# Performance work log

Measured on AMD Instinct MI355X. Metric: run time of the kernel, lower is better.

## Reference

```python
import jax, jax.numpy as jnp
import numpy as np

N, B, NUM_NODES, D_IN = 16384, 16, 1024, 1024
H, C = 4, 128
E = 262144


def _g(k, shape, fan_in):
    return jax.random.normal(k, shape, jnp.float32) * (1.0 / np.sqrt(fan_in))


def setup_inputs() -> dict:
    key = jax.random.key(0)
    ks = jax.random.split(key, 32)
    HC = H * C
    inp = {
        'x': jax.random.normal(ks[0], (N, D_IN), jnp.float32),
        'edge_index': jax.random.randint(ks[1], (2, E), 0, N, dtype=jnp.int64),
        'batch': jnp.repeat(jnp.arange(B, dtype=jnp.int64), NUM_NODES),
        # GATConv 1 (D_IN -> H x C, concat)
        'W1': _g(ks[2], (D_IN, HC), D_IN),
        'att_src1': _g(ks[3], (H, C), C),
        'att_dst1': _g(ks[4], (H, C), C),
        'b1': jnp.zeros((HC,), jnp.float32),
        # GATConv 2 (H*C -> H x C, concat)
        'W2': _g(ks[5], (HC, HC), HC),
        'att_src2': _g(ks[6], (H, C), C),
        'att_dst2': _g(ks[7], (H, C), C),
        'b2': jnp.zeros((HC,), jnp.float32),
        # pooling linears (HC -> 1)
        'p1w': _g(ks[8], (HC, 1), HC), 'p1b': jnp.zeros((1,), jnp.float32),
        'p2w': _g(ks[9], (HC, 1), HC), 'p2b': jnp.zeros((1,), jnp.float32),
        # layer_norm0 (applied to x2 per original code)
        'ln_g': jnp.ones((NUM_NODES,), jnp.float32),
        'ln_b': jnp.zeros((NUM_NODES,), jnp.float32),
        # encoder MLP 1024->512->256->128->64, last 64->1
        'fw1': _g(ks[10], (NUM_NODES, 512), NUM_NODES), 'fb1': jnp.zeros((512,), jnp.float32),
        'fw2': _g(ks[11], (512, 256), 512), 'fb2': jnp.zeros((256,), jnp.float32),
        'fw3': _g(ks[12], (256, 128), 256), 'fb3': jnp.zeros((128,), jnp.float32),
        'fw4': _g(ks[13], (128, 64), 128), 'fb4': jnp.zeros((64,), jnp.float32),
        'lw': _g(ks[14], (64, 1), 64), 'lb': jnp.zeros((1,), jnp.float32),
    }
    return inp


def gat_conv(x, src, dst, W, a_src, a_dst, b):
    # x: [N, F_in] -> h: [N, H, C]
    h = (x @ W).reshape(N, H, C)
    alpha_src = jnp.sum(h * a_src[None], axis=-1)  # [N, H]
    alpha_dst = jnp.sum(h * a_dst[None], axis=-1)  # [N, H]
    e = jax.nn.leaky_relu(alpha_src[src] + alpha_dst[dst], 0.2)  # [E', H]
    # segment softmax over destination neighborhoods (every node has a self loop)
    emax = jax.ops.segment_max(e, dst, num_segments=N)
    ex = jnp.exp(e - emax[dst])
    denom = jax.ops.segment_sum(ex, dst, num_segments=N)
    alpha = ex / (denom[dst] + 1e-16)  # [E', H]
    msg = h[src] * alpha[:, :, None]  # [E', H, C]
    out = jax.ops.segment_sum(msg, dst, num_segments=N)  # [N, H, C]
    return out.reshape(N, H * C) + b


def layer_norm(x, g, b, eps=1e-5):
    mu = jnp.mean(x, axis=-1, keepdims=True)
    var = jnp.var(x, axis=-1, keepdims=True)
    return (x - mu) * jax.lax.rsqrt(var + eps) * g + b


def reference(x, edge_index, batch, W1, att_src1, att_dst1, b1, W2, att_src2, att_dst2, b2,
              p1w, p1b, p2w, p2b, ln_g, ln_b, fw1, fb1, fw2, fb2, fw3, fb3, fw4, fb4, lw, lb):
    # add self loops (GATConv default)
    loops = jnp.arange(N, dtype=edge_index.dtype)
    src = jnp.concatenate([edge_index[0], loops])
    dst = jnp.concatenate([edge_index[1], loops])

    h1 = jax.nn.elu(gat_conv(x, src, dst, W1, att_src1, att_dst1, b1))
    # pool1 + to_dense_batch: batch is sorted with NUM_NODES nodes per graph -> reshape
    x1 = (h1 @ p1w + p1b).squeeze(-1).reshape(B, NUM_NODES)
    h2 = jax.nn.elu(gat_conv(h1, src, dst, W2, att_src2, att_dst2, b2))
    x2 = (h2 @ p2w + p2b).squeeze(-1).reshape(B, NUM_NODES)

    # opt.layer_norm=True; original bug: x2 normalized by layer_norm0
    x2 = layer_norm(x2, ln_g, ln_b)
    multiscale = x2  # which_layer == 'layer3'

    e = jax.nn.elu(multiscale @ fw1 + fb1)
    e = jax.nn.elu(e @ fw2 + fb2)
    e = jax.nn.elu(e @ fw3 + fb3)
    e = jax.nn.elu(e @ fw4 + fb4)
    pred = e @ lw + lb  # act_type='none' -> no activation
    return multiscale, e, pred
```

## Files before the change

kernel.cpp:

```cpp
#include <hip/hip_runtime.h>
#include <math.h>

#define NN    16384
#define DIN   1024
#define HCdim 512
#define NHEAD 4
#define NE_   262144
#define EP_   (NE_ + NN)

using short8  = __attribute__((ext_vector_type(8))) short;
using floatx4 = __attribute__((ext_vector_type(4))) float;

typedef __attribute__((address_space(3))) unsigned int lds_uint;
typedef const __attribute__((address_space(1))) unsigned int glb_uint;
#define ASYNC_LD16(g, l) __builtin_amdgcn_global_load_lds((glb_uint*)(g), (lds_uint*)(l), 16, 0, 0)

__device__ __forceinline__ float eluf(float x){ return x > 0.f ? x : expm1f(x); }
__device__ __forceinline__ float lrelu(float x){ return x > 0.f ? x : 0.2f * x; }
__device__ __forceinline__ float bf2f(unsigned short u){
    union { unsigned int i; float f; } c; c.i = ((unsigned int)u) << 16; return c.f;
}
__device__ __forceinline__ unsigned short f2b(float f){
    union { float f; unsigned int u; } c; c.f = f;
    unsigned int u = c.u;
    return (unsigned short)((u + 0x7FFFu + ((u >> 16) & 1u)) >> 16);
}

__global__ void k_zero_i(int* __restrict__ p, int n){
    int i = blockIdx.x * 256 + threadIdx.x;
    if (i < n) p[i] = 0;
}

__global__ void k_degree(const int* __restrict__ ei, int* __restrict__ deg){
    int i = blockIdx.x * 256 + threadIdx.x;
    if (i >= EP_) return;
    int d = (i < NE_) ? ei[NE_ + i] : (i - NE_);
    atomicAdd(&deg[d], 1);
}

__global__ __launch_bounds__(1024) void k_scan(const int* __restrict__ deg, int* __restrict__ offs){
    __shared__ int s[1024];
    int tid  = threadIdx.x;
    int base = tid * 16;
    int local[16];
    int sum = 0;
    #pragma unroll
    for (int i = 0; i < 16; i++){ local[i] = deg[base + i]; sum += local[i]; }
    s[tid] = sum;
    __syncthreads();
    for (int off = 1; off < 1024; off <<= 1){
        int v = (tid >= off) ? s[tid - off] : 0;
        __syncthreads();
        s[tid] += v;
        __syncthreads();
    }
    int run = (tid == 0) ? 0 : s[tid - 1];
    #pragma unroll
    for (int i = 0; i < 16; i++){ offs[base + i] = run; run += local[i]; }
    if (tid == 1023) offs[NN] = run;
}

__global__ void k_scatter(const int* __restrict__ ei, const int* __restrict__ offs,
                          int* __restrict__ cursor, int* __restrict__ csr){
    int i = blockIdx.x * 256 + threadIdx.x;
    if (i >= EP_) return;
    int srcv, dstv;
    if (i < NE_){ srcv = ei[i]; dstv = ei[NE_ + i]; }
    else        { srcv = dstv = i - NE_; }
    int pos = offs[dstv] + atomicAdd(&cursor[dstv], 1);
    csr[pos] = srcv;
}

__global__ __launch_bounds__(256) void k_casts(const float* __restrict__ x, ushort* __restrict__ xb,
    const float* __restrict__ W1, ushort* __restrict__ W1T,
    const float* __restrict__ W2, ushort* __restrict__ W2T){
    int bid = blockIdx.x, tid = threadIdx.x;
    if (bid < 16384){
        int i = bid * 256 + tid;
        float4 v = *(const float4*)(x + (size_t)i * 4);
        ushort4 o = { f2b(v.x), f2b(v.y), f2b(v.z), f2b(v.w) };
        *(ushort4*)(xb + (size_t)i * 4) = o;
    } else if (bid < 16384 + 512){
        int t = (bid - 16384) * 256 + tid;
        int n = t >> 8, kb = (t & 255) * 4;
        ushort4 o = { f2b(W1[(size_t)(kb+0)*HCdim + n]), f2b(W1[(size_t)(kb+1)*HCdim + n]),
                      f2b(W1[(size_t)(kb+2)*HCdim + n]), f2b(W1[(size_t)(kb+3)*HCdim + n]) };
        *(ushort4*)(W1T + (size_t)n * DIN + kb) = o;
    } else {
        int t = (bid - 16896) * 256 + tid;
        int n = t >> 7, kb = (t & 127) * 4;
        ushort4 o = { f2b(W2[(size_t)(kb+0)*HCdim + n]), f2b(W2[(size_t)(kb+1)*HCdim + n]),
                      f2b(W2[(size_t)(kb+2)*HCdim + n]), f2b(W2[(size_t)(kb+3)*HCdim + n]) };
        *(ushort4*)(W2T + (size_t)n * HCdim + kb) = o;
    }
}

__global__ __launch_bounds__(256) void gemm_bf16(const ushort* __restrict__ A,
                                                 const ushort* __restrict__ BT,
                                                 ushort* __restrict__ C,
                                                 const float* __restrict__ att_s,
                                                 const float* __restrict__ att_d,
                                                 float* __restrict__ as_, float* __restrict__ ad_,
                                                 int M, int Nn, int K){
    __shared__ ushort As[128 * 32];
    __shared__ ushort Bs[128 * 32];
    __shared__ float prS[2][128];
    __shared__ float prD[2][128];
    int tid = threadIdx.x;
    int m0 = blockIdx.y * 128, n0 = blockIdx.x * 128;
    int cx = blockIdx.x;
    int lane = tid & 63, w = tid >> 6;
    int wm = (w >> 1) * 64, wn = (w & 1) * 64;
    int la = lane & 15, qd = lane >> 4;

    int srow = tid >> 2, schunk = (tid & 3) * 8;
    const ushort* Ag = A  + (size_t)(m0 + srow) * K + schunk;
    const ushort* Bg = BT + (size_t)(n0 + srow) * K + schunk;
    ushort* Asw = &As[srow * 32 + schunk];
    ushort* Bsw = &Bs[srow * 32 + schunk];

    floatx4 acc[4][4] = {};
    for (int k0 = 0; k0 < K; k0 += 32){
        __syncthreads();
        ASYNC_LD16(Ag + k0,                  Asw);
        ASYNC_LD16(Ag + (size_t)64 * K + k0, Asw + 64 * 32);
        ASYNC_LD16(Bg + k0,                  Bsw);
        ASYNC_LD16(Bg + (size_t)64 * K + k0, Bsw + 64 * 32);
        __syncthreads();
        short8 af[4], bf[4];
        #pragma unroll
        for (int i = 0; i < 4; i++){
            af[i] = *(const short8*)&As[(wm + i*16 + la) * 32 + qd * 8];
            bf[i] = *(const short8*)&Bs[(wn + i*16 + la) * 32 + qd * 8];
        }
        #pragma unroll
        for (int i = 0; i < 4; i++)
            #pragma unroll
            for (int j = 0; j < 4; j++)
                acc[i][j] = __builtin_amdgcn_mfma_f32_16x16x32_bf16(af[i], bf[j], acc[i][j], 0, 0, 0);
    }
    float asv[4], adv[4];
    #pragma unroll
    for (int j = 0; j < 4; j++){
        asv[j] = att_s[cx * 128 + wn + j * 16 + la];
        adv[j] = att_d[cx * 128 + wn + j * 16 + la];
    }
    int half = wn >> 6;
    #pragma unroll
    for (int i = 0; i < 4; i++){
        #pragma unroll
        for (int r = 0; r < 4; r++){
            float ps = 0.f, pd = 0.f;
            #pragma unroll
            for (int j = 0; j < 4; j++){
                ps = fmaf(acc[i][j][r], asv[j], ps);
                pd = fmaf(acc[i][j][r], adv[j], pd);
            }
            #pragma unroll
            for (int off = 1; off < 16; off <<= 1){
                ps += __shfl_xor(ps, off);
                pd += __shfl_xor(pd, off);
            }
            if (la == 0){
                int rl = wm + i * 16 + qd * 4 + r;
                prS[half][rl] = ps; prD[half][rl] = pd;
            }
        }
    }
    #pragma unroll
    for (int i = 0; i < 4; i++)
        #pragma unroll
        for (int j = 0; j < 4; j++){
            int col = n0 + wn + j * 16 + la;
            #pragma unroll
            for (int r = 0; r < 4; r++){
                int row = m0 + wm + i * 16 + qd * 4 + r;
                C[(size_t)row * Nn + col] = f2b(acc[i][j][r]);
            }
        }
    __syncthreads();
    if (tid < 128){
        as_[(size_t)(m0 + tid) * 4 + cx] = prS[0][tid] + prS[1][tid];
        ad_[(size_t)(m0 + tid) * 4 + cx] = prD[0][tid] + prD[1][tid];
    }
}

__global__ __launch_bounds__(256) void k_edgew(const int* __restrict__ offs, const int* __restrict__ csr,
    const float* __restrict__ as_, const float* __restrict__ ad_, ushort* __restrict__ wbuf){
    int wv = threadIdx.x >> 6, lane = threadIdx.x & 63;
    int n = blockIdx.x * 4 + wv;
    int start = offs[n], end = offs[n + 1];
    float4 ad4 = *(const float4*)(ad_ + (size_t)n * 4);
    for (int j = start + lane; j < end; j += 64){
        int s = csr[j];
        float4 as4 = *(const float4*)(as_ + (size_t)s * 4);
        ushort4 o = { f2b(__expf(lrelu(as4.x + ad4.x))), f2b(__expf(lrelu(as4.y + ad4.y))),
                      f2b(__expf(lrelu(as4.z + ad4.z))), f2b(__expf(lrelu(as4.w + ad4.w))) };
        *(ushort4*)(wbuf + (size_t)j * 4) = o;
    }
}

#define AGG_CONSUME(WS, HV)                                  \
    { float wgt = bf2f(WS);                                  \
      dsum += wgt;                                           \
      a0 = fmaf(wgt, bf2f(HV.x & 0xffff), a0);               \
      a1 = fmaf(wgt, bf2f(HV.x >> 16),    a1);               \
      a2 = fmaf(wgt, bf2f(HV.y & 0xffff), a2);               \
      a3 = fmaf(wgt, bf2f(HV.y >> 16),    a3);               \
      a4 = fmaf(wgt, bf2f(HV.z & 0xffff), a4);               \
      a5 = fmaf(wgt, bf2f(HV.z >> 16),    a5);               \
      a6 = fmaf(wgt, bf2f(HV.w & 0xffff), a6);               \
      a7 = fmaf(wgt, bf2f(HV.w >> 16),    a7); }

template<bool POOL>
__global__ __launch_bounds__(256) void k_aggregate(const ushort* __restrict__ h,
    const int* __restrict__ offs, const int* __restrict__ csr,
    const ushort* __restrict__ wbuf,
    const float* __restrict__ bias, ushort* __restrict__ out,
    const float* __restrict__ pw, const float* __restrict__ pb, float* __restrict__ x2){
    int wv   = threadIdx.x >> 6;
    int lane = threadIdx.x & 63;
    int n    = blockIdx.x * 4 + wv;
    int head = lane >> 4;
    int start = offs[n], end = offs[n + 1];
    float dsum = 0.f;
    float a0=0.f,a1=0.f,a2=0.f,a3=0.f,a4=0.f,a5=0.f,a6=0.f,a7=0.f;
    for (int base = start; base < end; base += 64){
        int cnt = min(64, end - base);
        int pre = (base + lane < end) ? csr[base + lane] : 0;
        int s0 = __builtin_amdgcn_readlane(pre, 0);
        ushort w0 = wbuf[(size_t)base * 4 + head];
        uint4  h0 = *(const uint4*)(h + (size_t)s0 * HCdim + lane * 8);
        ushort w1 = 0; uint4 h1 = {0,0,0,0};
        if (cnt > 1){
            int s1 = __builtin_amdgcn_readlane(pre, 1);
            w1 = wbuf[(size_t)(base + 1) * 4 + head];
            h1 = *(const uint4*)(h + (size_t)s1 * HCdim + lane * 8);
        }
        for (int jj = 0; jj < cnt; jj++){
            ushort w2 = 0; uint4 h2 = {0,0,0,0};
            if (jj + 2 < cnt){
                int s2 = __builtin_amdgcn_readlane(pre, jj + 2);
                w2 = wbuf[(size_t)(base + jj + 2) * 4 + head];
                h2 = *(const uint4*)(h + (size_t)s2 * HCdim + lane * 8);
            }
            AGG_CONSUME(w0, h0);
            w0 = w1; h0 = h1;
            w1 = w2; h1 = h2;
        }
    }
    float rden = 1.f / (dsum + 1e-16f);
    float4 b0 = *(const float4*)(bias + lane * 8);
    float4 b1 = *(const float4*)(bias + lane * 8 + 4);
    float e0 = eluf(fmaf(a0, rden, b0.x));
    float e1 = eluf(fmaf(a1, rden, b0.y));
    float e2 = eluf(fmaf(a2, rden, b0.z));
    float e3 = eluf(fmaf(a3, rden, b0.w));
    float e4 = eluf(fmaf(a4, rden, b1.x));
    float e5 = eluf(fmaf(a5, rden, b1.y));
    float e6 = eluf(fmaf(a6, rden, b1.z));
    float e7 = eluf(fmaf(a7, rden, b1.w));
    uint4 o;
    o.x = (unsigned)f2b(e0) | ((unsigned)f2b(e1) << 16);
    o.y = (unsigned)f2b(e2) | ((unsigned)f2b(e3) << 16);
    o.z = (unsigned)f2b(e4) | ((unsigned)f2b(e5) << 16);
    o.w = (unsigned)f2b(e6) | ((unsigned)f2b(e7) << 16);
    *(uint4*)(out + (size_t)n * HCdim + lane * 8) = o;
    if (POOL){
        float4 w0p = *(const float4*)(pw + lane * 8);
        float4 w1p = *(const float4*)(pw + lane * 8 + 4);
        float s = e0*w0p.x + e1*w0p.y + e2*w0p.z + e3*w0p.w
                + e4*w1p.x + e5*w1p.y + e6*w1p.z + e7*w1p.w;
        #pragma unroll
        for (int off = 32; off; off >>= 1) s += __shfl_down(s, off);
        if (lane == 0) x2[n] = s + pb[0];
    }
}

__global__ __launch_bounds__(256) void k_fc1_ln(const float* __restrict__ x2,
    const float* __restrict__ lng, const float* __restrict__ lnb,
    const float* __restrict__ W, const float* __restrict__ bias,
    float* __restrict__ outms, float* __restrict__ e1b){
    __shared__ float xs[1024];
    __shared__ float red[4][64];
    __shared__ float red2[8];
    __shared__ float stats[2];
    int tid = threadIdx.x;
    int b = blockIdx.y, c0 = blockIdx.x * 64;
    float4 v = *(const float4*)(x2 + b * 1024 + tid * 4);
    float s  = v.x + v.y + v.z + v.w;
    float sq = v.x * v.x + v.y * v.y + v.z * v.z + v.w * v.w;
    #pragma unroll
    for (int off = 32; off; off >>= 1){ s += __shfl_down(s, off); sq += __shfl_down(sq, off); }
    if ((tid & 63) == 0){ red2[(tid >> 6) * 2] = s; red2[(tid >> 6) * 2 + 1] = sq; }
    __syncthreads();
    if (tid == 0){
        float S  = red2[0] + red2[2] + red2[4] + red2[6];
        float SQ = red2[1] + red2[3] + red2[5] + red2[7];
        float mu  = S * (1.f / 1024.f);
        float var = SQ * (1.f / 1024.f) - mu * mu;
        stats[0] = mu; stats[1] = rsqrtf(var + 1e-5f);
    }
    __syncthreads();
    float mu = stats[0], r = stats[1];
    float4 g4  = *(const float4*)(lng + tid * 4);
    float4 bb4 = *(const float4*)(lnb + tid * 4);
    float4 o;
    o.x = (v.x - mu) * r * g4.x + bb4.x;
    o.y = (v.y - mu) * r * g4.y + bb4.y;
    o.z = (v.z - mu) * r * g4.z + bb4.z;
    o.w = (v.w - mu) * r * g4.w + bb4.w;
    *(float4*)&xs[tid * 4] = o;
    if (blockIdx.x == 0) *(float4*)(outms + b * 1024 + tid * 4) = o;
    __syncthreads();
    int tx = tid & 63, ty = tid >> 6;
    const float* wp = W + (size_t)(ty * 256) * 512 + c0 + tx;
    float a = 0.f;
    #pragma unroll 8
    for (int i = 0; i < 256; i++)
        a = fmaf(xs[ty * 256 + i], wp[(size_t)i * 512], a);
    red[ty][tx] = a;
    __syncthreads();
    if (ty == 0){
        float vv = red[0][tx] + red[1][tx] + red[2][tx] + red[3][tx] + bias[c0 + tx];
        e1b[b * 512 + c0 + tx] = eluf(vv);
    }
}

template<int K, int NOUT>
__global__ __launch_bounds__(256) void k_fc(const float* __restrict__ in,
    const float* __restrict__ W, const float* __restrict__ bias, float* __restrict__ outb){
    __shared__ float xs[K];
    __shared__ float red[4][64];
    int tid = threadIdx.x;
    int b = blockIdx.y, c0 = blockIdx.x * 64;
    int tx = tid & 63, ty = tid >> 6;
    for (int i = tid * 4; i < K; i += 1024)
        *(float4*)&xs[i] = *(const float4*)(in + b * K + i);
    __syncthreads();
    const float* wp = W + (size_t)(ty * (K / 4)) * NOUT + c0 + tx;
    float a = 0.f;
    #pragma unroll 8
    for (int i = 0; i < K / 4; i++)
        a = fmaf(xs[ty * (K / 4) + i], wp[(size_t)i * NOUT], a);
    red[ty][tx] = a;
    __syncthreads();
    if (ty == 0){
        float v = red[0][tx] + red[1][tx] + red[2][tx] + red[3][tx] + bias[c0 + tx];
        outb[b * NOUT + tx + c0] = eluf(v);
    }
}

__global__ __launch_bounds__(256) void k_fc_final(const float* __restrict__ in,
    const float* __restrict__ W, const float* __restrict__ bias,
    const float* __restrict__ lw, const float* __restrict__ lb, float* __restrict__ out){
    __shared__ float xs[128];
    __shared__ float red[4][64];
    __shared__ float evs[64];
    int tid = threadIdx.x;
    int b = blockIdx.x;
    int tx = tid & 63, ty = tid >> 6;
    if (tid * 4 < 128)
        *(float4*)&xs[tid * 4] = *(const float4*)(in + b * 128 + tid * 4);
    __syncthreads();
    const float* wp = W + (size_t)(ty * 32) * 64 + tx;
    float a = 0.f;
    #pragma unroll
    for (int i = 0; i < 32; i++)
        a = fmaf(xs[ty * 32 + i], wp[(size_t)i * 64], a);
    red[ty][tx] = a;
    __syncthreads();
    if (ty == 0){
        float ev = eluf(red[0][tx] + red[1][tx] + red[2][tx] + red[3][tx] + bias[tx]);
        evs[tx] = ev;
        out[16384 + b * 64 + tx] = ev;
    }
    __syncthreads();
    if (ty == 0){
        float p = evs[tx] * lw[tx];
        #pragma unroll
        for (int off = 32; off; off >>= 1) p += __shfl_down(p, off);
        if (tx == 0) out[16384 + 1024 + b] = p + lb[0];
    }
}

extern "C" void kernel_launch(void* const* d_in, const int* in_sizes, int n_in,
                              void* d_out, int out_size, void* d_ws, size_t ws_size,
                              hipStream_t stream) {
    const float* x        = (const float*)d_in[0];
    const int*   ei       = (const int*)  d_in[1];
    const float* W1       = (const float*)d_in[3];
    const float* att_src1 = (const float*)d_in[4];
    const float* att_dst1 = (const float*)d_in[5];
    const float* b1       = (const float*)d_in[6];
    const float* W2       = (const float*)d_in[7];
    const float* att_src2 = (const float*)d_in[8];
    const float* att_dst2 = (const float*)d_in[9];
    const float* b2       = (const float*)d_in[10];
    const float* p2w      = (const float*)d_in[13];
    const float* p2b      = (const float*)d_in[14];
    const float* ln_g     = (const float*)d_in[15];
    const float* ln_b     = (const float*)d_in[16];
    const float* fw1      = (const float*)d_in[17];
    const float* fb1      = (const float*)d_in[18];
    const float* fw2      = (const float*)d_in[19];
    const float* fb2      = (const float*)d_in[20];
    const float* fw3      = (const float*)d_in[21];
    const float* fb3      = (const float*)d_in[22];
    const float* fw4      = (const float*)d_in[23];
    const float* fb4      = (const float*)d_in[24];
    const float* lw       = (const float*)d_in[25];
    const float* lb       = (const float*)d_in[26];
    float* out = (float*)d_out;

    char* w = (char*)d_ws;
    ushort* xb   = (ushort*)(w);
    ushort* h1b  = (ushort*)(w);
    ushort* h2b  = (ushort*)(w + 16777216);
    ushort* hpre = (ushort*)(w + 33554432);
    ushort* W1T  = (ushort*)(w + 50331648);
    ushort* W2T  = (ushort*)(w + 51380224);
    float* asb   = (float*)(w + 51904512);
    float* adb   = (float*)(w + 52166656);
    int*   deg   = (int*)  (w + 52428800);
    int*   cursor= (int*)  (w + 52494336);
    int*   offs  = (int*)  (w + 52559872);
    int*   csr   = (int*)  (w + 52625664);
    ushort* wbuf = (ushort*)(w + 53739776);
    float* x2b   = (float*)(w + 55968000);
    float* e1b   = (float*)(w + 56033536);
    float* e2b   = (float*)(w + 56066304);
    float* e3b   = (float*)(w + 56082688);

    k_zero_i <<<(2 * NN + 255) / 256, 256, 0, stream>>>(deg, 2 * NN);
    k_degree <<<(EP_ + 255) / 256, 256, 0, stream>>>(ei, deg);
    k_scan   <<<1, 1024, 0, stream>>>(deg, offs);
    k_scatter<<<(EP_ + 255) / 256, 256, 0, stream>>>(ei, offs, cursor, csr);

    k_casts<<<16384 + 512 + 256, 256, 0, stream>>>(x, xb, W1, W1T, W2, W2T);

    dim3 ggrid(HCdim / 128, NN / 128);
    gemm_bf16         <<<ggrid, 256, 0, stream>>>(xb, W1T, hpre, att_src1, att_dst1,
                                                  asb, adb, NN, HCdim, DIN);
    k_edgew           <<<NN / 4, 256, 0, stream>>>(offs, csr, asb, adb, wbuf);
    k_aggregate<false><<<NN / 4, 256, 0, stream>>>(hpre, offs, csr, wbuf, b1, h1b,
                                                   nullptr, nullptr, nullptr);
    gemm_bf16         <<<ggrid, 256, 0, stream>>>(h1b, W2T, hpre, att_src2, att_dst2,
                                                  asb, adb, NN, HCdim, HCdim);
    k_edgew           <<<NN / 4, 256, 0, stream>>>(offs, csr, asb, adb, wbuf);
    k_aggregate<true> <<<NN / 4, 256, 0, stream>>>(hpre, offs, csr, wbuf, b2, h2b,
                                                   p2w, p2b, x2b);
    k_fc1_ln          <<<dim3(8, 16), 256, 0, stream>>>(x2b, ln_g, ln_b, fw1, fb1, out, e1b);
    k_fc< 512, 256>   <<<dim3(4, 16), 256, 0, stream>>>(e1b, fw2, fb2, e2b);
    k_fc< 256, 128>   <<<dim3(2, 16), 256, 0, stream>>>(e2b, fw3, fb3, e3b);
    k_fc_final        <<<16, 256, 0, stream>>>(e3b, fw4, fb4, lw, lb, out);
}
```

Before: 376.0 us.

## Split aggregation rows across two waves and deepen gather prefetch to eight edges

The GAT aggregation kernel now assigns two wavefronts per destination node, each covering half the 512 channels with 4 channels per lane, which doubles the grid. The gather loop is restructured into a double-buffered pipeline that keeps 4 to 8 neighbor loads in flight instead of 2. Out-of-range edges are clamped and given zero weight rather than branched around. The pooling reduction now combines the two half-row partials through shared memory with a block barrier. The aim is more memory-level parallelism for the irregular neighbor gathers, at the cost of narrower 8-byte loads and duplicated CSR and weight reads per node.

```diff
diff --git a/kernel.cpp b/kernel.cpp
--- a/kernel.cpp
+++ b/kernel.cpp
@@ -200,80 +200,75 @@
     }
 }
 
-#define AGG_CONSUME(WS, HV)                                  \
-    { float wgt = bf2f(WS);                                  \
-      dsum += wgt;                                           \
-      a0 = fmaf(wgt, bf2f(HV.x & 0xffff), a0);               \
-      a1 = fmaf(wgt, bf2f(HV.x >> 16),    a1);               \
-      a2 = fmaf(wgt, bf2f(HV.y & 0xffff), a2);               \
-      a3 = fmaf(wgt, bf2f(HV.y >> 16),    a3);               \
-      a4 = fmaf(wgt, bf2f(HV.z & 0xffff), a4);               \
-      a5 = fmaf(wgt, bf2f(HV.z >> 16),    a5);               \
-      a6 = fmaf(wgt, bf2f(HV.w & 0xffff), a6);               \
-      a7 = fmaf(wgt, bf2f(HV.w >> 16),    a7); }
-
 template<bool POOL>
 __global__ __launch_bounds__(256) void k_aggregate(const ushort* __restrict__ h,
     const int* __restrict__ offs, const int* __restrict__ csr,
     const ushort* __restrict__ wbuf,
     const float* __restrict__ bias, ushort* __restrict__ out,
     const float* __restrict__ pw, const float* __restrict__ pb, float* __restrict__ x2){
+    __shared__ float pr[4];
     int wv   = threadIdx.x >> 6;
     int lane = threadIdx.x & 63;
-    int n    = blockIdx.x * 4 + wv;
-    int head = lane >> 4;
+    int n    = blockIdx.x * 2 + (wv >> 1);
+    int half = wv & 1;
+    int cb   = half * 256 + lane * 4;
+    int head = cb >> 7;
     int start = offs[n], end = offs[n + 1];
+    const ushort* hrow = h + cb;
+    const ushort* wrow = wbuf + head;
     float dsum = 0.f;
-    float a0=0.f,a1=0.f,a2=0.f,a3=0.f,a4=0.f,a5=0.f,a6=0.f,a7=0.f;
+    float a0 = 0.f, a1 = 0.f, a2 = 0.f, a3 = 0.f;
+
     for (int base = start; base < end; base += 64){
         int cnt = min(64, end - base);
-        int pre = (base + lane < end) ? csr[base + lane] : 0;
-        int s0 = __builtin_amdgcn_readlane(pre, 0);
-        ushort w0 = wbuf[(size_t)base * 4 + head];
-        uint4  h0 = *(const uint4*)(h + (size_t)s0 * HCdim + lane * 8);
-        ushort w1 = 0; uint4 h1 = {0,0,0,0};
-        if (cnt > 1){
-            int s1 = __builtin_amdgcn_readlane(pre, 1);
-            w1 = wbuf[(size_t)(base + 1) * 4 + head];
-            h1 = *(const uint4*)(h + (size_t)s1 * HCdim + lane * 8);
+        int pre = csr[base + min(lane, cnt - 1)];
+        float wa0, wa1, wa2, wa3, wb0, wb1, wb2, wb3;
+        uint2 ha0, ha1, ha2, ha3, hb0, hb1, hb2, hb3;
+
+#define LOADE(W, H, E)                                                        \
+        { int e_ = (E); int ec_ = min(e_, cnt - 1);                           \
+          int s_ = __builtin_amdgcn_readlane(pre, ec_);                       \
+          float wv_ = bf2f(wrow[(size_t)(base + ec_) * 4]);                   \
+          W = (e_ < cnt) ? wv_ : 0.f;                                         \
+          H = *(const uint2*)(hrow + (size_t)s_ * HCdim); }
+
+#define CONS(W, H)                                                            \
+        { dsum += W;                                                          \
+          a0 = fmaf(W, bf2f(H.x & 0xffff), a0);                               \
+          a1 = fmaf(W, bf2f(H.x >> 16),    a1);                               \
+          a2 = fmaf(W, bf2f(H.y & 0xffff), a2);                               \
+          a3 = fmaf(W, bf2f(H.y >> 16),    a3); }
+
+        LOADE(wa0, ha0, 0) LOADE(wa1, ha1, 1) LOADE(wa2, ha2, 2) LOADE(wa3, ha3, 3)
+        for (int g = 0; g < cnt; g += 8){
+            LOADE(wb0, hb0, g + 4) LOADE(wb1, hb1, g + 5)
+            LOADE(wb2, hb2, g + 6) LOADE(wb3, hb3, g + 7)
+            CONS(wa0, ha0) CONS(wa1, ha1) CONS(wa2, ha2) CONS(wa3, ha3)
+            LOADE(wa0, ha0, g + 8) LOADE(wa1, ha1, g + 9)
+            LOADE(wa2, ha2, g + 10) LOADE(wa3, ha3, g + 11)
+            CONS(wb0, hb0) CONS(wb1, hb1) CONS(wb2, hb2) CONS(wb3, hb3)
         }
-        for (int jj = 0; jj < cnt; jj++){
-            ushort w2 = 0; uint4 h2 = {0,0,0,0};
-            if (jj + 2 < cnt){
-                int s2 = __builtin_amdgcn_readlane(pre, jj + 2);
-                w2 = wbuf[(size_t)(base + jj + 2) * 4 + head];
-                h2 = *(const uint4*)(h + (size_t)s2 * HCdim + lane * 8);
-            }
-            AGG_CONSUME(w0, h0);
-            w0 = w1; h0 = h1;
-            w1 = w2; h1 = h2;
-        }
+#undef LOADE
+#undef CONS
     }
     float rden = 1.f / (dsum + 1e-16f);
-    float4 b0 = *(const float4*)(bias + lane * 8);
-    float4 b1 = *(const float4*)(bias + lane * 8 + 4);
-    float e0 = eluf(fmaf(a0, rden, b0.x));
-    float e1 = eluf(fmaf(a1, rden, b0.y));
-    float e2 = eluf(fmaf(a2, rden, b0.z));
-    float e3 = eluf(fmaf(a3, rden, b0.w));
-    float e4 = eluf(fmaf(a4, rden, b1.x));
-    float e5 = eluf(fmaf(a5, rden, b1.y));
-    float e6 = eluf(fmaf(a6, rden, b1.z));
-    float e7 = eluf(fmaf(a7, rden, b1.w));
-    uint4 o;
+    float4 b4 = *(const float4*)(bias + cb);
+    float e0 = eluf(fmaf(a0, rden, b4.x));
+    float e1 = eluf(fmaf(a1, rden, b4.y));
+    float e2 = eluf(fmaf(a2, rden, b4.z));
+    float e3 = eluf(fmaf(a3, rden, b4.w));
+    uint2 o;
     o.x = (unsigned)f2b(e0) | ((unsigned)f2b(e1) << 16);
     o.y = (unsigned)f2b(e2) | ((unsigned)f2b(e3) << 16);
-    o.z = (unsigned)f2b(e4) | ((unsigned)f2b(e5) << 16);
-    o.w = (unsigned)f2b(e6) | ((unsigned)f2b(e7) << 16);
-    *(uint4*)(out + (size_t)n * HCdim + lane * 8) = o;
+    *(uint2*)(out + (size_t)n * HCdim + cb) = o;
     if (POOL){
-        float4 w0p = *(const float4*)(pw + lane * 8);
-        float4 w1p = *(const float4*)(pw + lane * 8 + 4);
-        float s = e0*w0p.x + e1*w0p.y + e2*w0p.z + e3*w0p.w
-                + e4*w1p.x + e5*w1p.y + e6*w1p.z + e7*w1p.w;
+        float4 w4 = *(const float4*)(pw + cb);
+        float s = e0 * w4.x + e1 * w4.y + e2 * w4.z + e3 * w4.w;
         #pragma unroll
         for (int off = 32; off; off >>= 1) s += __shfl_down(s, off);
-        if (lane == 0) x2[n] = s + pb[0];
+        if (lane == 0) pr[wv] = s;
+        __syncthreads();
+        if (half == 0 && lane == 0) x2[n] = pr[wv] + pr[wv + 1] + pb[0];
     }
 }
 
@@ -443,12 +438,12 @@
     gemm_bf16         <<<ggrid, 256, 0, stream>>>(xb, W1T, hpre, att_src1, att_dst1,
                                                   asb, adb, NN, HCdim, DIN);
     k_edgew           <<<NN / 4, 256, 0, stream>>>(offs, csr, asb, adb, wbuf);
-    k_aggregate<false><<<NN / 4, 256, 0, stream>>>(hpre, offs, csr, wbuf, b1, h1b,
+    k_aggregate<false><<<NN / 2, 256, 0, stream>>>(hpre, offs, csr, wbuf, b1, h1b,
                                                    nullptr, nullptr, nullptr);
     gemm_bf16         <<<ggrid, 256, 0, stream>>>(h1b, W2T, hpre, att_src2, att_dst2,
                                                   asb, adb, NN, HCdim, HCdim);
     k_edgew           <<<NN / 4, 256, 0, stream>>>(offs, csr, asb, adb, wbuf);
-    k_aggregate<true> <<<NN / 4, 256, 0, stream>>>(hpre, offs, csr, wbuf, b2, h2b,
+    k_aggregate<true> <<<NN / 2, 256, 0, stream>>>(hpre, offs, csr, wbuf, b2, h2b,
                                                    p2w, p2b, x2b);
     k_fc1_ln          <<<dim3(8, 16), 256, 0, stream>>>(x2b, ln_g, ln_b, fw1, fb1, out, e1b);
     k_fc< 512, 256>   <<<dim3(4, 16), 256, 0, stream>>>(e1b, fw2, fb2, e2b);
```

Result: no change. 371.0 us (-1.3%).

## Deepen aggregate gather pipeline to 8 in flight; fuse MLP tail into one kernel

Applied to the files above, without the earlier changes.

The neighbour-aggregation loop now keeps two groups of four edge loads in flight (ping-pong A/B registers) instead of a 2-deep prefetch. Out-of-range edges are clamped to a valid index and given zero weight, which removes per-edge branches. The three small MLP-tail kernels (fc2, fc3, fc4 plus the final projection) are merged into one 16-block kernel that keeps intermediates in LDS, saving two launches and their global round trips. The cost is higher register pressure in the aggregate kernel and redundant loads on padded edges.

```diff
diff --git a/kernel.cpp b/kernel.cpp
--- a/kernel.cpp
+++ b/kernel.cpp
@@ -200,18 +200,6 @@
     }
 }
 
-#define AGG_CONSUME(WS, HV)                                  \
-    { float wgt = bf2f(WS);                                  \
-      dsum += wgt;                                           \
-      a0 = fmaf(wgt, bf2f(HV.x & 0xffff), a0);               \
-      a1 = fmaf(wgt, bf2f(HV.x >> 16),    a1);               \
-      a2 = fmaf(wgt, bf2f(HV.y & 0xffff), a2);               \
-      a3 = fmaf(wgt, bf2f(HV.y >> 16),    a3);               \
-      a4 = fmaf(wgt, bf2f(HV.z & 0xffff), a4);               \
-      a5 = fmaf(wgt, bf2f(HV.z >> 16),    a5);               \
-      a6 = fmaf(wgt, bf2f(HV.w & 0xffff), a6);               \
-      a7 = fmaf(wgt, bf2f(HV.w >> 16),    a7); }
-
 template<bool POOL>
 __global__ __launch_bounds__(256) void k_aggregate(const ushort* __restrict__ h,
     const int* __restrict__ offs, const int* __restrict__ csr,
@@ -221,37 +209,52 @@
     int wv   = threadIdx.x >> 6;
     int lane = threadIdx.x & 63;
     int n    = blockIdx.x * 4 + wv;
+    int cb   = lane * 8;
     int head = lane >> 4;
     int start = offs[n], end = offs[n + 1];
+    const ushort* hrow = h + cb;
     float dsum = 0.f;
     float a0=0.f,a1=0.f,a2=0.f,a3=0.f,a4=0.f,a5=0.f,a6=0.f,a7=0.f;
+
     for (int base = start; base < end; base += 64){
-        int cnt = min(64, end - base);
-        int pre = (base + lane < end) ? csr[base + lane] : 0;
-        int s0 = __builtin_amdgcn_readlane(pre, 0);
-        ushort w0 = wbuf[(size_t)base * 4 + head];
-        uint4  h0 = *(const uint4*)(h + (size_t)s0 * HCdim + lane * 8);
-        ushort w1 = 0; uint4 h1 = {0,0,0,0};
-        if (cnt > 1){
-            int s1 = __builtin_amdgcn_readlane(pre, 1);
-            w1 = wbuf[(size_t)(base + 1) * 4 + head];
-            h1 = *(const uint4*)(h + (size_t)s1 * HCdim + lane * 8);
+        int bcnt = min(64, end - base);
+        int pre = csr[base + min(lane, bcnt - 1)];
+        float wA0, wA1, wA2, wA3, wB0, wB1, wB2, wB3;
+        uint4 hA0, hA1, hA2, hA3, hB0, hB1, hB2, hB3;
+
+#define LOADE(W, H, E)                                                        \
+        { int e_ = (E); int ec_ = min(e_, bcnt - 1);                          \
+          int s_ = __builtin_amdgcn_readlane(pre, ec_);                       \
+          float wv_ = bf2f(wbuf[(size_t)(base + ec_) * 4 + head]);            \
+          W = (e_ < bcnt) ? wv_ : 0.f;                                        \
+          H = *(const uint4*)(hrow + (size_t)s_ * HCdim); }
+
+#define CONS(W, H)                                                            \
+        { dsum += W;                                                          \
+          a0 = fmaf(W, bf2f(H.x & 0xffff), a0);                               \
+          a1 = fmaf(W, bf2f(H.x >> 16),    a1);                               \
+          a2 = fmaf(W, bf2f(H.y & 0xffff), a2);                               \
+          a3 = fmaf(W, bf2f(H.y >> 16),    a3);                               \
+          a4 = fmaf(W, bf2f(H.z & 0xffff), a4);                               \
+          a5 = fmaf(W, bf2f(H.z >> 16),    a5);                               \
+          a6 = fmaf(W, bf2f(H.w & 0xffff), a6);                               \
+          a7 = fmaf(W, bf2f(H.w >> 16),    a7); }
+
+        LOADE(wA0, hA0, 0) LOADE(wA1, hA1, 1) LOADE(wA2, hA2, 2) LOADE(wA3, hA3, 3)
+        for (int g = 0; g < bcnt; g += 8){
+            LOADE(wB0, hB0, g + 4) LOADE(wB1, hB1, g + 5)
+            LOADE(wB2, hB2, g + 6) LOADE(wB3, hB3, g + 7)
+            CONS(wA0, hA0) CONS(wA1, hA1) CONS(wA2, hA2) CONS(wA3, hA3)
+            LOADE(wA0, hA0, g + 8) LOADE(wA1, hA1, g + 9)
+            LOADE(wA2, hA2, g + 10) LOADE(wA3, hA3, g + 11)
+            CONS(wB0, hB0) CONS(wB1, hB1) CONS(wB2, hB2) CONS(wB3, hB3)
         }
-        for (int jj = 0; jj < cnt; jj++){
-            ushort w2 = 0; uint4 h2 = {0,0,0,0};
-            if (jj + 2 < cnt){
-                int s2 = __builtin_amdgcn_readlane(pre, jj + 2);
-                w2 = wbuf[(size_t)(base + jj + 2) * 4 + head];
-                h2 = *(const uint4*)(h + (size_t)s2 * HCdim + lane * 8);
-            }
-            AGG_CONSUME(w0, h0);
-            w0 = w1; h0 = h1;
-            w1 = w2; h1 = h2;
-        }
+#undef LOADE
+#undef CONS
     }
     float rden = 1.f / (dsum + 1e-16f);
-    float4 b0 = *(const float4*)(bias + lane * 8);
-    float4 b1 = *(const float4*)(bias + lane * 8 + 4);
+    float4 b0 = *(const float4*)(bias + cb);
+    float4 b1 = *(const float4*)(bias + cb + 4);
     float e0 = eluf(fmaf(a0, rden, b0.x));
     float e1 = eluf(fmaf(a1, rden, b0.y));
     float e2 = eluf(fmaf(a2, rden, b0.z));
@@ -265,10 +268,10 @@
     o.y = (unsigned)f2b(e2) | ((unsigned)f2b(e3) << 16);
     o.z = (unsigned)f2b(e4) | ((unsigned)f2b(e5) << 16);
     o.w = (unsigned)f2b(e6) | ((unsigned)f2b(e7) << 16);
-    *(uint4*)(out + (size_t)n * HCdim + lane * 8) = o;
+    *(uint4*)(out + (size_t)n * HCdim + cb) = o;
     if (POOL){
-        float4 w0p = *(const float4*)(pw + lane * 8);
-        float4 w1p = *(const float4*)(pw + lane * 8 + 4);
+        float4 w0p = *(const float4*)(pw + cb);
+        float4 w1p = *(const float4*)(pw + cb + 4);
         float s = e0*w0p.x + e1*w0p.y + e2*w0p.z + e3*w0p.w
                 + e4*w1p.x + e5*w1p.y + e6*w1p.z + e7*w1p.w;
         #pragma unroll
@@ -327,60 +330,42 @@
     }
 }
 
-template<int K, int NOUT>
-__global__ __launch_bounds__(256) void k_fc(const float* __restrict__ in,
-    const float* __restrict__ W, const float* __restrict__ bias, float* __restrict__ outb){
-    __shared__ float xs[K];
-    __shared__ float red[4][64];
-    int tid = threadIdx.x;
-    int b = blockIdx.y, c0 = blockIdx.x * 64;
-    int tx = tid & 63, ty = tid >> 6;
-    for (int i = tid * 4; i < K; i += 1024)
-        *(float4*)&xs[i] = *(const float4*)(in + b * K + i);
-    __syncthreads();
-    const float* wp = W + (size_t)(ty * (K / 4)) * NOUT + c0 + tx;
-    float a = 0.f;
+__global__ __launch_bounds__(256) void k_mlp_tail(const float* __restrict__ e1b,
+    const float* __restrict__ fw2, const float* __restrict__ fb2,
+    const float* __restrict__ fw3, const float* __restrict__ fb3,
+    const float* __restrict__ fw4, const float* __restrict__ fb4,
+    const float* __restrict__ lw,  const float* __restrict__ lb,
+    float* __restrict__ out){
+    __shared__ float s1[512];
+    __shared__ float s2[256];
+    __shared__ float s3[128];
+    __shared__ float evs[64];
+    int b = blockIdx.x, tid = threadIdx.x;
+    *(float2*)&s1[tid * 2] = *(const float2*)(e1b + b * 512 + tid * 2);
+    __syncthreads();
+    float a = fb2[tid];
     #pragma unroll 8
-    for (int i = 0; i < K / 4; i++)
-        a = fmaf(xs[ty * (K / 4) + i], wp[(size_t)i * NOUT], a);
-    red[ty][tx] = a;
-    __syncthreads();
-    if (ty == 0){
-        float v = red[0][tx] + red[1][tx] + red[2][tx] + red[3][tx] + bias[c0 + tx];
-        outb[b * NOUT + tx + c0] = eluf(v);
-    }
-}
-
-__global__ __launch_bounds__(256) void k_fc_final(const float* __restrict__ in,
-    const float* __restrict__ W, const float* __restrict__ bias,
-    const float* __restrict__ lw, const float* __restrict__ lb, float* __restrict__ out){
-    __shared__ float xs[128];
-    __shared__ float red[4][64];
-    __shared__ float evs[64];
-    int tid = threadIdx.x;
-    int b = blockIdx.x;
-    int tx = tid & 63, ty = tid >> 6;
-    if (tid * 4 < 128)
-        *(float4*)&xs[tid * 4] = *(const float4*)(in + b * 128 + tid * 4);
-    __syncthreads();
-    const float* wp = W + (size_t)(ty * 32) * 64 + tx;
-    float a = 0.f;
-    #pragma unroll
-    for (int i = 0; i < 32; i++)
-        a = fmaf(xs[ty * 32 + i], wp[(size_t)i * 64], a);
-    red[ty][tx] = a;
-    __syncthreads();
-    if (ty == 0){
-        float ev = eluf(red[0][tx] + red[1][tx] + red[2][tx] + red[3][tx] + bias[tx]);
-        evs[tx] = ev;
-        out[16384 + b * 64 + tx] = ev;
-    }
-    __syncthreads();
-    if (ty == 0){
-        float p = evs[tx] * lw[tx];
+    for (int i = 0; i < 512; i++) a = fmaf(s1[i], fw2[i * 256 + tid], a);
+    s2[tid] = eluf(a);
+    __syncthreads();
+    if (tid < 128){
+        float a3 = fb3[tid];
+        #pragma unroll 8
+        for (int i = 0; i < 256; i++) a3 = fmaf(s2[i], fw3[i * 128 + tid], a3);
+        s3[tid] = eluf(a3);
+    }
+    __syncthreads();
+    if (tid < 64){
+        float a4 = fb4[tid];
+        #pragma unroll 8
+        for (int i = 0; i < 128; i++) a4 = fmaf(s3[i], fw4[i * 64 + tid], a4);
+        float ev = eluf(a4);
+        evs[tid] = ev;
+        out[16384 + b * 64 + tid] = ev;
+        float p = ev * lw[tid];
         #pragma unroll
         for (int off = 32; off; off >>= 1) p += __shfl_down(p, off);
-        if (tx == 0) out[16384 + 1024 + b] = p + lb[0];
+        if (tid == 0) out[16384 + 1024 + b] = p + lb[0];
     }
 }
 
@@ -429,8 +414,6 @@
     ushort* wbuf = (ushort*)(w + 53739776);
     float* x2b   = (float*)(w + 55968000);
     float* e1b   = (float*)(w + 56033536);
-    float* e2b   = (float*)(w + 56066304);
-    float* e3b   = (float*)(w + 56082688);
 
     k_zero_i <<<(2 * NN + 255) / 256, 256, 0, stream>>>(deg, 2 * NN);
     k_degree <<<(EP_ + 255) / 256, 256, 0, stream>>>(ei, deg);
@@ -451,7 +434,5 @@
     k_aggregate<true> <<<NN / 4, 256, 0, stream>>>(hpre, offs, csr, wbuf, b2, h2b,
                                                    p2w, p2b, x2b);
     k_fc1_ln          <<<dim3(8, 16), 256, 0, stream>>>(x2b, ln_g, ln_b, fw1, fb1, out, e1b);
-    k_fc< 512, 256>   <<<dim3(4, 16), 256, 0, stream>>>(e1b, fw2, fb2, e2b);
-    k_fc< 256, 128>   <<<dim3(2, 16), 256, 0, stream>>>(e2b, fw3, fb3, e3b);
-    k_fc_final        <<<16, 256, 0, stream>>>(e3b, fw4, fb4, lw, lb, out);
-}
+    k_mlp_tail        <<<16, 256, 0, stream>>>(e1b, fw2, fb2, fw3, fb3, fw4, fb4, lw, lb, out);
+}
```

New measurement: 404.7 us. +7.6%, slower.

## Quantize GAT projected features to int8 with per-head row scales for aggregation

Applied to the files above, without the earlier changes.

The GEMM epilogue now swaps MFMA operands to get a transposed accumulator layout and computes per-row, per-head absmax. It writes the projected features as int8 with a scale, instead of bf16. The edge-weight kernel folds that scale into a second bf16 weight packed alongside the softmax weight. The aggregation kernel gathers half the bytes per neighbor, using 8-edge software pipelining. Layer 2 no longer writes h2 since only the pooled output is needed. The gather traffic drops, at the cost of int8 quantization error in the attention-weighted features.

```diff
diff --git a/kernel.cpp b/kernel.cpp
--- a/kernel.cpp
+++ b/kernel.cpp
@@ -97,15 +97,17 @@
 
 __global__ __launch_bounds__(256) void gemm_bf16(const ushort* __restrict__ A,
                                                  const ushort* __restrict__ BT,
-                                                 ushort* __restrict__ C,
+                                                 signed char* __restrict__ C,
                                                  const float* __restrict__ att_s,
                                                  const float* __restrict__ att_d,
                                                  float* __restrict__ as_, float* __restrict__ ad_,
+                                                 float* __restrict__ sclb,
                                                  int M, int Nn, int K){
     __shared__ ushort As[128 * 32];
     __shared__ ushort Bs[128 * 32];
     __shared__ float prS[2][128];
     __shared__ float prD[2][128];
+    __shared__ float amx[2][128];
     int tid = threadIdx.x;
     int m0 = blockIdx.y * 128, n0 = blockIdx.x * 128;
     int cx = blockIdx.x;
@@ -137,56 +139,66 @@
         for (int i = 0; i < 4; i++)
             #pragma unroll
             for (int j = 0; j < 4; j++)
-                acc[i][j] = __builtin_amdgcn_mfma_f32_16x16x32_bf16(af[i], bf[j], acc[i][j], 0, 0, 0);
-    }
-    float asv[4], adv[4];
+                acc[i][j] = __builtin_amdgcn_mfma_f32_16x16x32_bf16(bf[i], af[j], acc[i][j], 0, 0, 0);
+    }
+    float4 s4[4], d4[4];
+    #pragma unroll
+    for (int i = 0; i < 4; i++){
+        s4[i] = *(const float4*)(att_s + cx * 128 + wn + i * 16 + qd * 4);
+        d4[i] = *(const float4*)(att_d + cx * 128 + wn + i * 16 + qd * 4);
+    }
+    int half = wn >> 6;
     #pragma unroll
     for (int j = 0; j < 4; j++){
-        asv[j] = att_s[cx * 128 + wn + j * 16 + la];
-        adv[j] = att_d[cx * 128 + wn + j * 16 + la];
-    }
-    int half = wn >> 6;
-    #pragma unroll
-    for (int i = 0; i < 4; i++){
-        #pragma unroll
-        for (int r = 0; r < 4; r++){
-            float ps = 0.f, pd = 0.f;
-            #pragma unroll
-            for (int j = 0; j < 4; j++){
-                ps = fmaf(acc[i][j][r], asv[j], ps);
-                pd = fmaf(acc[i][j][r], adv[j], pd);
-            }
-            #pragma unroll
-            for (int off = 1; off < 16; off <<= 1){
-                ps += __shfl_xor(ps, off);
-                pd += __shfl_xor(pd, off);
-            }
-            if (la == 0){
-                int rl = wm + i * 16 + qd * 4 + r;
-                prS[half][rl] = ps; prD[half][rl] = pd;
-            }
-        }
-    }
-    #pragma unroll
-    for (int i = 0; i < 4; i++)
-        #pragma unroll
-        for (int j = 0; j < 4; j++){
-            int col = n0 + wn + j * 16 + la;
-            #pragma unroll
-            for (int r = 0; r < 4; r++){
-                int row = m0 + wm + i * 16 + qd * 4 + r;
-                C[(size_t)row * Nn + col] = f2b(acc[i][j][r]);
-            }
-        }
-    __syncthreads();
+        float ps = 0.f, pd = 0.f;
+        #pragma unroll
+        for (int i = 0; i < 4; i++){
+            ps = fmaf(acc[i][j][0], s4[i].x, ps); pd = fmaf(acc[i][j][0], d4[i].x, pd);
+            ps = fmaf(acc[i][j][1], s4[i].y, ps); pd = fmaf(acc[i][j][1], d4[i].y, pd);
+            ps = fmaf(acc[i][j][2], s4[i].z, ps); pd = fmaf(acc[i][j][2], d4[i].z, pd);
+            ps = fmaf(acc[i][j][3], s4[i].w, ps); pd = fmaf(acc[i][j][3], d4[i].w, pd);
+        }
+        ps += __shfl_xor(ps, 16); ps += __shfl_xor(ps, 32);
+        pd += __shfl_xor(pd, 16); pd += __shfl_xor(pd, 32);
+        float am = 0.f;
+        #pragma unroll
+        for (int i = 0; i < 4; i++){
+            am = fmaxf(am, fabsf(acc[i][j][0])); am = fmaxf(am, fabsf(acc[i][j][1]));
+            am = fmaxf(am, fabsf(acc[i][j][2])); am = fmaxf(am, fabsf(acc[i][j][3]));
+        }
+        am = fmaxf(am, __shfl_xor(am, 16)); am = fmaxf(am, __shfl_xor(am, 32));
+        if (lane < 16){
+            prS[half][wm + j * 16 + la] = ps;
+            prD[half][wm + j * 16 + la] = pd;
+            amx[half][wm + j * 16 + la] = am;
+        }
+    }
+    __syncthreads();
+    #pragma unroll
+    for (int j = 0; j < 4; j++){
+        int nl = wm + j * 16 + la;
+        float amax = fmaxf(fmaxf(amx[0][nl], amx[1][nl]), 1e-20f);
+        float inv = 127.0f / amax;
+        #pragma unroll
+        for (int i = 0; i < 4; i++){
+            int q0 = (int)rintf(acc[i][j][0] * inv);
+            int q1 = (int)rintf(acc[i][j][1] * inv);
+            int q2 = (int)rintf(acc[i][j][2] * inv);
+            int q3 = (int)rintf(acc[i][j][3] * inv);
+            unsigned pk = (q0 & 0xff) | ((q1 & 0xff) << 8) | ((q2 & 0xff) << 16) | ((q3 & 0xff) << 24);
+            *(unsigned*)(C + (size_t)(m0 + nl) * HCdim + n0 + wn + i * 16 + qd * 4) = pk;
+        }
+    }
     if (tid < 128){
-        as_[(size_t)(m0 + tid) * 4 + cx] = prS[0][tid] + prS[1][tid];
-        ad_[(size_t)(m0 + tid) * 4 + cx] = prD[0][tid] + prD[1][tid];
+        as_[(size_t)(m0 + tid) * 4 + cx]  = prS[0][tid] + prS[1][tid];
+        ad_[(size_t)(m0 + tid) * 4 + cx]  = prD[0][tid] + prD[1][tid];
+        sclb[(size_t)(m0 + tid) * 4 + cx] = fmaxf(fmaxf(amx[0][tid], amx[1][tid]), 1e-20f) * (1.f / 127.f);
     }
 }
 
 __global__ __launch_bounds__(256) void k_edgew(const int* __restrict__ offs, const int* __restrict__ csr,
-    const float* __restrict__ as_, const float* __restrict__ ad_, ushort* __restrict__ wbuf){
+    const float* __restrict__ as_, const float* __restrict__ ad_,
+    const float* __restrict__ sclb, unsigned* __restrict__ wbuf){
     int wv = threadIdx.x >> 6, lane = threadIdx.x & 63;
     int n = blockIdx.x * 4 + wv;
     int start = offs[n], end = offs[n + 1];
@@ -194,64 +206,81 @@
     for (int j = start + lane; j < end; j += 64){
         int s = csr[j];
         float4 as4 = *(const float4*)(as_ + (size_t)s * 4);
-        ushort4 o = { f2b(__expf(lrelu(as4.x + ad4.x))), f2b(__expf(lrelu(as4.y + ad4.y))),
-                      f2b(__expf(lrelu(as4.z + ad4.z))), f2b(__expf(lrelu(as4.w + ad4.w))) };
-        *(ushort4*)(wbuf + (size_t)j * 4) = o;
-    }
-}
-
-#define AGG_CONSUME(WS, HV)                                  \
-    { float wgt = bf2f(WS);                                  \
-      dsum += wgt;                                           \
-      a0 = fmaf(wgt, bf2f(HV.x & 0xffff), a0);               \
-      a1 = fmaf(wgt, bf2f(HV.x >> 16),    a1);               \
-      a2 = fmaf(wgt, bf2f(HV.y & 0xffff), a2);               \
-      a3 = fmaf(wgt, bf2f(HV.y >> 16),    a3);               \
-      a4 = fmaf(wgt, bf2f(HV.z & 0xffff), a4);               \
-      a5 = fmaf(wgt, bf2f(HV.z >> 16),    a5);               \
-      a6 = fmaf(wgt, bf2f(HV.w & 0xffff), a6);               \
-      a7 = fmaf(wgt, bf2f(HV.w >> 16),    a7); }
+        float4 sc4 = *(const float4*)(sclb + (size_t)s * 4);
+        float w0 = __expf(lrelu(as4.x + ad4.x));
+        float w1 = __expf(lrelu(as4.y + ad4.y));
+        float w2 = __expf(lrelu(as4.z + ad4.z));
+        float w3 = __expf(lrelu(as4.w + ad4.w));
+        uint4 o;
+        o.x = (unsigned)f2b(w0) | ((unsigned)f2b(w0 * sc4.x) << 16);
+        o.y = (unsigned)f2b(w1) | ((unsigned)f2b(w1 * sc4.y) << 16);
+        o.z = (unsigned)f2b(w2) | ((unsigned)f2b(w2 * sc4.z) << 16);
+        o.w = (unsigned)f2b(w3) | ((unsigned)f2b(w3 * sc4.w) << 16);
+        *(uint4*)(wbuf + (size_t)j * 4) = o;
+    }
+}
 
 template<bool POOL>
-__global__ __launch_bounds__(256) void k_aggregate(const ushort* __restrict__ h,
+__global__ __launch_bounds__(256) void k_aggregate(const signed char* __restrict__ h,
     const int* __restrict__ offs, const int* __restrict__ csr,
-    const ushort* __restrict__ wbuf,
+    const unsigned* __restrict__ wbuf,
     const float* __restrict__ bias, ushort* __restrict__ out,
     const float* __restrict__ pw, const float* __restrict__ pb, float* __restrict__ x2){
     int wv   = threadIdx.x >> 6;
     int lane = threadIdx.x & 63;
     int n    = blockIdx.x * 4 + wv;
+    int cb   = lane * 8;
     int head = lane >> 4;
     int start = offs[n], end = offs[n + 1];
+    const signed char* hrow = h + cb;
     float dsum = 0.f;
     float a0=0.f,a1=0.f,a2=0.f,a3=0.f,a4=0.f,a5=0.f,a6=0.f,a7=0.f;
+
     for (int base = start; base < end; base += 64){
-        int cnt = min(64, end - base);
-        int pre = (base + lane < end) ? csr[base + lane] : 0;
-        int s0 = __builtin_amdgcn_readlane(pre, 0);
-        ushort w0 = wbuf[(size_t)base * 4 + head];
-        uint4  h0 = *(const uint4*)(h + (size_t)s0 * HCdim + lane * 8);
-        ushort w1 = 0; uint4 h1 = {0,0,0,0};
-        if (cnt > 1){
-            int s1 = __builtin_amdgcn_readlane(pre, 1);
-            w1 = wbuf[(size_t)(base + 1) * 4 + head];
-            h1 = *(const uint4*)(h + (size_t)s1 * HCdim + lane * 8);
-        }
-        for (int jj = 0; jj < cnt; jj++){
-            ushort w2 = 0; uint4 h2 = {0,0,0,0};
-            if (jj + 2 < cnt){
-                int s2 = __builtin_amdgcn_readlane(pre, jj + 2);
-                w2 = wbuf[(size_t)(base + jj + 2) * 4 + head];
-                h2 = *(const uint4*)(h + (size_t)s2 * HCdim + lane * 8);
-            }
-            AGG_CONSUME(w0, h0);
-            w0 = w1; h0 = h1;
-            w1 = w2; h1 = h2;
-        }
+        int bcnt = min(64, end - base);
+        int pre = csr[base + min(lane, bcnt - 1)];
+        unsigned wA0, wA1, wA2, wA3, wB0, wB1, wB2, wB3;
+        uint2 hA0, hA1, hA2, hA3, hB0, hB1, hB2, hB3;
+
+#define LOADE(W, H, E)                                                        \
+        { int e_ = (E); int ec_ = min(e_, bcnt - 1);                          \
+          int s_ = __builtin_amdgcn_readlane(pre, ec_);                       \
+          unsigned wp_ = wbuf[(size_t)(base + ec_) * 4 + head];               \
+          W = (e_ < bcnt) ? wp_ : 0u;                                         \
+          H = *(const uint2*)(hrow + (size_t)s_ * HCdim); }
+
+#define CONS(W, H)                                                            \
+        { float w_  = bf2f((unsigned short)(W & 0xffff));                     \
+          float ws_ = bf2f((unsigned short)(W >> 16));                        \
+          dsum += w_;                                                         \
+          int q0 = (int)(H.x << 24) >> 24;                                    \
+          int q1 = (int)(H.x << 16) >> 24;                                    \
+          int q2 = (int)(H.x <<  8) >> 24;                                    \
+          int q3 = (int) H.x        >> 24;                                    \
+          int q4 = (int)(H.y << 24) >> 24;                                    \
+          int q5 = (int)(H.y << 16) >> 24;                                    \
+          int q6 = (int)(H.y <<  8) >> 24;                                    \
+          int q7 = (int) H.y        >> 24;                                    \
+          a0 = fmaf(ws_, (float)q0, a0); a1 = fmaf(ws_, (float)q1, a1);       \
+          a2 = fmaf(ws_, (float)q2, a2); a3 = fmaf(ws_, (float)q3, a3);       \
+          a4 = fmaf(ws_, (float)q4, a4); a5 = fmaf(ws_, (float)q5, a5);       \
+          a6 = fmaf(ws_, (float)q6, a6); a7 = fmaf(ws_, (float)q7, a7); }
+
+        LOADE(wA0, hA0, 0) LOADE(wA1, hA1, 1) LOADE(wA2, hA2, 2) LOADE(wA3, hA3, 3)
+        for (int g = 0; g < bcnt; g += 8){
+            LOADE(wB0, hB0, g + 4) LOADE(wB1, hB1, g + 5)
+            LOADE(wB2, hB2, g + 6) LOADE(wB3, hB3, g + 7)
+            CONS(wA0, hA0) CONS(wA1, hA1) CONS(wA2, hA2) CONS(wA3, hA3)
+            LOADE(wA0, hA0, g + 8) LOADE(wA1, hA1, g + 9)
+            LOADE(wA2, hA2, g + 10) LOADE(wA3, hA3, g + 11)
+            CONS(wB0, hB0) CONS(wB1, hB1) CONS(wB2, hB2) CONS(wB3, hB3)
+        }
+#undef LOADE
+#undef CONS
     }
     float rden = 1.f / (dsum + 1e-16f);
-    float4 b0 = *(const float4*)(bias + lane * 8);
-    float4 b1 = *(const float4*)(bias + lane * 8 + 4);
+    float4 b0 = *(const float4*)(bias + cb);
+    float4 b1 = *(const float4*)(bias + cb + 4);
     float e0 = eluf(fmaf(a0, rden, b0.x));
     float e1 = eluf(fmaf(a1, rden, b0.y));
     float e2 = eluf(fmaf(a2, rden, b0.z));
@@ -260,15 +289,16 @@
     float e5 = eluf(fmaf(a5, rden, b1.y));
     float e6 = eluf(fmaf(a6, rden, b1.z));
     float e7 = eluf(fmaf(a7, rden, b1.w));
-    uint4 o;
-    o.x = (unsigned)f2b(e0) | ((unsigned)f2b(e1) << 16);
-    o.y = (unsigned)f2b(e2) | ((unsigned)f2b(e3) << 16);
-    o.z = (unsigned)f2b(e4) | ((unsigned)f2b(e5) << 16);
-    o.w = (unsigned)f2b(e6) | ((unsigned)f2b(e7) << 16);
-    *(uint4*)(out + (size_t)n * HCdim + lane * 8) = o;
-    if (POOL){
-        float4 w0p = *(const float4*)(pw + lane * 8);
-        float4 w1p = *(const float4*)(pw + lane * 8 + 4);
+    if (!POOL){
+        uint4 o;
+        o.x = (unsigned)f2b(e0) | ((unsigned)f2b(e1) << 16);
+        o.y = (unsigned)f2b(e2) | ((unsigned)f2b(e3) << 16);
+        o.z = (unsigned)f2b(e4) | ((unsigned)f2b(e5) << 16);
+        o.w = (unsigned)f2b(e6) | ((unsigned)f2b(e7) << 16);
+        *(uint4*)(out + (size_t)n * HCdim + cb) = o;
+    } else {
+        float4 w0p = *(const float4*)(pw + cb);
+        float4 w1p = *(const float4*)(pw + cb + 4);
         float s = e0*w0p.x + e1*w0p.y + e2*w0p.z + e3*w0p.w
                 + e4*w1p.x + e5*w1p.y + e6*w1p.z + e7*w1p.w;
         #pragma unroll
@@ -416,21 +446,21 @@
     char* w = (char*)d_ws;
     ushort* xb   = (ushort*)(w);
     ushort* h1b  = (ushort*)(w);
-    ushort* h2b  = (ushort*)(w + 16777216);
-    ushort* hpre = (ushort*)(w + 33554432);
-    ushort* W1T  = (ushort*)(w + 50331648);
-    ushort* W2T  = (ushort*)(w + 51380224);
-    float* asb   = (float*)(w + 51904512);
-    float* adb   = (float*)(w + 52166656);
-    int*   deg   = (int*)  (w + 52428800);
-    int*   cursor= (int*)  (w + 52494336);
-    int*   offs  = (int*)  (w + 52559872);
-    int*   csr   = (int*)  (w + 52625664);
-    ushort* wbuf = (ushort*)(w + 53739776);
-    float* x2b   = (float*)(w + 55968000);
-    float* e1b   = (float*)(w + 56033536);
-    float* e2b   = (float*)(w + 56066304);
-    float* e3b   = (float*)(w + 56082688);
+    signed char* hpre = (signed char*)(w + 33554432);
+    ushort* W1T  = (ushort*)(w + 41943040);
+    ushort* W2T  = (ushort*)(w + 42991616);
+    float* asb   = (float*)(w + 43515904);
+    float* adb   = (float*)(w + 43778048);
+    float* sclb  = (float*)(w + 44040192);
+    int*   deg   = (int*)  (w + 44302336);
+    int*   cursor= (int*)  (w + 44367872);
+    int*   offs  = (int*)  (w + 44433408);
+    int*   csr   = (int*)  (w + 44499200);
+    unsigned* wbuf = (unsigned*)(w + 45613312);
+    float* x2b   = (float*)(w + 50069760);
+    float* e1b   = (float*)(w + 50135296);
+    float* e2b   = (float*)(w + 50167808);
+    float* e3b   = (float*)(w + 50184192);
 
     k_zero_i <<<(2 * NN + 255) / 256, 256, 0, stream>>>(deg, 2 * NN);
     k_degree <<<(EP_ + 255) / 256, 256, 0, stream>>>(ei, deg);
@@ -441,14 +471,14 @@
 
     dim3 ggrid(HCdim / 128, NN / 128);
     gemm_bf16         <<<ggrid, 256, 0, stream>>>(xb, W1T, hpre, att_src1, att_dst1,
-                                                  asb, adb, NN, HCdim, DIN);
-    k_edgew           <<<NN / 4, 256, 0, stream>>>(offs, csr, asb, adb, wbuf);
+                                                  asb, adb, sclb, NN, HCdim, DIN);
+    k_edgew           <<<NN / 4, 256, 0, stream>>>(offs, csr, asb, adb, sclb, wbuf);
     k_aggregate<false><<<NN / 4, 256, 0, stream>>>(hpre, offs, csr, wbuf, b1, h1b,
                                                    nullptr, nullptr, nullptr);
     gemm_bf16         <<<ggrid, 256, 0, stream>>>(h1b, W2T, hpre, att_src2, att_dst2,
-                                                  asb, adb, NN, HCdim, HCdim);
-    k_edgew           <<<NN / 4, 256, 0, stream>>>(offs, csr, asb, adb, wbuf);
-    k_aggregate<true> <<<NN / 4, 256, 0, stream>>>(hpre, offs, csr, wbuf, b2, h2b,
+                                                  asb, adb, sclb, NN, HCdim, HCdim);
+    k_edgew           <<<NN / 4, 256, 0, stream>>>(offs, csr, asb, adb, sclb, wbuf);
+    k_aggregate<true> <<<NN / 4, 256, 0, stream>>>(hpre, offs, csr, wbuf, b2, nullptr,
                                                    p2w, p2b, x2b);
     k_fc1_ln          <<<dim3(8, 16), 256, 0, stream>>>(x2b, ln_g, ln_b, fw1, fb1, out, e1b);
     k_fc< 512, 256>   <<<dim3(4, 16), 256, 0, stream>>>(e1b, fw2, fb2, e2b);
```

Result: faster. 350.2 us (-6.9%).
